# Optimization experiments

Hardware: AMD Instinct MI355X
Metric: run time of the kernel (lower is better)

Reference implementation:

```python
import jax, jax.numpy as jnp
import numpy as np
from jax import lax

DIM = 256
HEADS = 8
EPS = 1e-12  # torch F.normalize default eps
DN = ('NCHW', 'OIHW', 'NCHW')


def conv1x1(x, w):
    return lax.conv_general_dilated(x, w, (1, 1), 'VALID', dimension_numbers=DN)


def dwconv3x3(x, w):
    c = x.shape[1]
    return lax.conv_general_dilated(x, w, (1, 1), ((1, 1), (1, 1)),
                                    dimension_numbers=DN, feature_group_count=c)


def setup_inputs() -> dict:
    key = jax.random.key(0)
    ks = jax.random.split(key, 8)
    B, C, H, W = 4, DIM, 160, 160
    s = lambda fan: 1.0 / np.sqrt(fan)
    return {
        'low': jax.random.normal(ks[0], (B, C, H, W), jnp.float32),
        'high': jax.random.normal(ks[1], (B, C, H, W), jnp.float32),
        'q_w': jax.random.normal(ks[2], (C, C, 1, 1), jnp.float32) * s(C),
        'q_dw_w': jax.random.normal(ks[3], (C, 1, 3, 3), jnp.float32) * s(9),
        'kv_w': jax.random.normal(ks[4], (2 * C, C, 1, 1), jnp.float32) * s(C),
        'kv_dw_w': jax.random.normal(ks[5], (2 * C, 1, 3, 3), jnp.float32) * s(9),
        'proj_w': jax.random.normal(ks[6], (C, C, 1, 1), jnp.float32) * s(C),
        'temperature': jnp.ones((HEADS, 1, 1), jnp.float32),
    }


def reference(low, high, q_w, q_dw_w, kv_w, kv_dw_w, proj_w, temperature):
    B, C, H, W = low.shape
    hw = H * W
    ch = C // HEADS  # channels per head

    q = dwconv3x3(conv1x1(high, q_w), q_dw_w)           # [B, C, H, W]
    kv = dwconv3x3(conv1x1(low, kv_w), kv_dw_w)         # [B, 2C, H, W]
    k, v = jnp.split(kv, 2, axis=1)

    def heads(x):
        return x.reshape(B, HEADS, ch, hw)              # b head c (h w)

    q, k, v = heads(q), heads(k), heads(v)

    # L2-normalize along spatial dim (torch F.normalize semantics)
    q = q / jnp.maximum(jnp.linalg.norm(q, axis=-1, keepdims=True), EPS)
    k = k / jnp.maximum(jnp.linalg.norm(k, axis=-1, keepdims=True), EPS)

    attn = jnp.einsum('bhcn,bhdn->bhcd', q, k) * temperature  # [B, H, ch, ch]
    attn = jax.nn.softmax(attn, axis=-1)
    out = jnp.einsum('bhcd,bhdn->bhcn', attn, v)               # [B, H, ch, hw]

    out = out.reshape(B, C, H, W)
    return conv1x1(out, proj_w)
```

## Files before the change

kernel.cpp:

```cpp
#include <hip/hip_runtime.h>
#include <math.h>

#define HW 25600
#define IMGW 160
#define CDIM 256
#define NB 4
#define NHEADS 8
#define SZB ((long)CDIM * HW)

typedef __attribute__((ext_vector_type(8))) short short8v;
typedef __attribute__((ext_vector_type(4))) float f32x4;
typedef __attribute__((ext_vector_type(8))) unsigned short us8;

union FragU {
    us8 o;
    short8v s;
    unsigned u32[4];
};

__device__ inline unsigned short f2bf(float f) {
    unsigned u = __float_as_uint(f);
    return (unsigned short)((u + 0x7fffu + ((u >> 16) & 1u)) >> 16);
}
__device__ inline float bf2f(unsigned short h) {
    return __uint_as_float(((unsigned)h) << 16);
}

__global__ __launch_bounds__(256) void cvtw_k(
    const float* __restrict__ kv_w, const float* __restrict__ q_w,
    unsigned short* __restrict__ wkv_s, unsigned short* __restrict__ wq_s)
{
    int idx = blockIdx.x * 256 + threadIdx.x;
    int g2 = idx & 3;
    int kt = (idx >> 2) & 7;
    int co = idx >> 5;
    const float* src;
    unsigned short* dst;
    int nco, co_l;
    if (co < 512) { src = kv_w; dst = wkv_s; nco = 512; co_l = co; }
    else          { src = q_w;  dst = wq_s;  nco = 256; co_l = co - 512; }
    src += (long)co_l * CDIM + kt * 32 + g2 * 8;
    us8 v;
#pragma unroll
    for (int u = 0; u < 8; ++u) v[u] = f2bf(src[u]);
    int slot = g2 ^ ((co_l >> 1) & 3);
    *(us8*)(dst + ((long)kt * nco + co_l) * 32 + slot * 8) = v;
}

template<int OUTF32, int XF32>
__global__ __launch_bounds__(256) void gemm2_k(
    const void* __restrict__ Xv, const unsigned short* __restrict__ WS,
    void* __restrict__ outp, long xbs, long wbs, long obs, int nco)
{
    __shared__ __align__(16) unsigned short Wl[128 * 32];
    __shared__ __align__(16) char XBuf[XF32 ? (128 * 40 * 2) : (128 * 32 * 2)];
    unsigned short* Xl = (unsigned short*)XBuf;

    const int t  = threadIdx.x;
    const int l  = t & 63;
    const int wv = t >> 6;
    const int g  = l >> 4;
    const int ln = l & 15;

    const int NX = gridDim.x;
    const int orig = blockIdx.y * NX + blockIdx.x;
    const int chunkp = (NX * gridDim.y) >> 3;
    const int wgid = (orig & 7) * chunkp + (orig >> 3);
    const int co0 = (wgid % NX) * 128;
    const int n0  = (wgid / NX) * 128;

    const long b  = blockIdx.z;
    const unsigned short* Wb = WS + b * wbs;
    const int wr = wv >> 1, wc = wv & 1;

    f32x4 acc[4][4];
#pragma unroll
    for (int i = 0; i < 4; ++i)
#pragma unroll
        for (int j = 0; j < 4; ++j) acc[i][j] = (f32x4){0.f, 0.f, 0.f, 0.f};

    const int lrow = l >> 2;
    const int lgrp = l & 3;
    const int n_l = t & 127;
    const int sb  = (t >> 7) * 2;

    for (int kt = 0; kt < 8; ++kt) {
        __syncthreads();
#pragma unroll
        for (int ii = 0; ii < 2; ++ii) {
            int instr = wv * 2 + ii;
            int row = instr * 16 + lrow;
            const unsigned short* wsrc =
                Wb + ((long)kt * nco + co0 + row) * 32 + lgrp * 8;
            __builtin_amdgcn_global_load_lds(
                (const __attribute__((address_space(1))) void*)wsrc,
                (__attribute__((address_space(3))) void*)&Wl[instr * 512], 16, 0, 0);
        }
        if (XF32) {
            const float* Xb = (const float*)Xv + b * xbs;
#pragma unroll
            for (int si = 0; si < 2; ++si) {
                int k0 = (sb + si) * 8;
                float f[8];
#pragma unroll
                for (int u = 0; u < 8; ++u)
                    f[u] = Xb[(long)(kt * 32 + k0 + u) * HW + n0 + n_l];
                FragU cv;
#pragma unroll
                for (int e2 = 0; e2 < 4; ++e2) {
                    unsigned r;
                    asm("v_cvt_pk_bf16_f32 %0, %1, %2"
                        : "=v"(r) : "v"(f[e2 * 2]), "v"(f[e2 * 2 + 1]));
                    cv.u32[e2] = r;
                }
                *(us8*)&Xl[n_l * 40 + k0] = cv.o;
            }
        } else {
            const unsigned short* Xb = (const unsigned short*)Xv + b * xbs;
#pragma unroll
            for (int ii = 0; ii < 2; ++ii) {
                int instr = wv * 2 + ii;
                int row = instr * 16 + lrow;
                const unsigned short* xsrc =
                    Xb + ((long)kt * HW + n0 + row) * 32 + lgrp * 8;
                __builtin_amdgcn_global_load_lds(
                    (const __attribute__((address_space(1))) void*)xsrc,
                    (__attribute__((address_space(3))) void*)&Xl[instr * 512], 16, 0, 0);
            }
        }
        __syncthreads();

        FragU A_[4], B_[4];
#pragma unroll
        for (int i = 0; i < 4; ++i) {
            int row = wr * 64 + i * 16 + ln;
            int slot = g ^ ((row >> 1) & 3);
            A_[i].o = *(const us8*)&Wl[row * 32 + slot * 8];
        }
        if (XF32) {
#pragma unroll
            for (int j = 0; j < 4; ++j) {
                int row = wc * 64 + j * 16 + ln;
                B_[j].o = *(const us8*)&Xl[row * 40 + g * 8];
            }
        } else {
#pragma unroll
            for (int j = 0; j < 4; ++j) {
                int row = wc * 64 + j * 16 + ln;
                int slot = g ^ ((row >> 1) & 3);
                B_[j].o = *(const us8*)&Xl[row * 32 + slot * 8];
            }
        }
#pragma unroll
        for (int i = 0; i < 4; ++i)
#pragma unroll
            for (int j = 0; j < 4; ++j)
                acc[i][j] = __builtin_amdgcn_mfma_f32_16x16x32_bf16(
                    A_[i].s, B_[j].s, acc[i][j], 0, 0, 0);
    }

    if (OUTF32) {
        float* ob = (float*)outp + b * obs;
#pragma unroll
        for (int i = 0; i < 4; ++i)
#pragma unroll
            for (int j = 0; j < 4; ++j) {
                long ocol = n0 + wc * 64 + j * 16 + ln;
#pragma unroll
                for (int r = 0; r < 4; ++r) {
                    long orow = co0 + wr * 64 + i * 16 + g * 4 + r;
                    ob[orow * HW + ocol] = acc[i][j][r];
                }
            }
    } else {
        unsigned short* ob = (unsigned short*)outp + b * obs;
#pragma unroll
        for (int i = 0; i < 4; ++i)
#pragma unroll
            for (int j = 0; j < 4; ++j) {
                long ocol = n0 + wc * 64 + j * 16 + ln;
#pragma unroll
                for (int r = 0; r < 4; ++r) {
                    long orow = co0 + wr * 64 + i * 16 + g * 4 + r;
                    ob[orow * HW + ocol] = f2bf(acc[i][j][r]);
                }
            }
    }
}

__global__ __launch_bounds__(256) void dwK_k(
    const unsigned short* __restrict__ A, const float* __restrict__ w,
    unsigned short* __restrict__ out, long bstride)
{
    __shared__ unsigned short xsh[8][10][168];
    const int t = threadIdx.x;
    const int y0 = blockIdx.x * 8;
    const int c0 = blockIdx.y * 8;
    const long b = blockIdx.z;
    const unsigned short* Ab = A + b * bstride;

    for (int idx = t; idx < 1600; idx += 256) {
        int seg = idx % 20;
        int row = (idx / 20) % 10;
        int ch  = idx / 200;
        int yy  = y0 + row - 1;
        us8 v = (us8){0, 0, 0, 0, 0, 0, 0, 0};
        if (yy >= 0 && yy < IMGW)
            v = *(const us8*)(Ab + (long)(c0 + ch) * HW + yy * IMGW + seg * 8);
        *(us8*)&xsh[ch][row][seg * 8] = v;
    }
    __syncthreads();

    const int ch = t >> 5;
    const int rem = t & 31;
    const int ro = rem >> 2;
    const int xq = rem & 3;
    float wreg[9];
#pragma unroll
    for (int u = 0; u < 9; ++u) wreg[u] = w[(c0 + ch) * 9 + u];
    unsigned short* ob = out + b * SZB + (long)(c0 + ch) * HW + (y0 + ro) * IMGW;

#pragma unroll
    for (int xs = 0; xs < 5; ++xs) {
        int x = xq * 8 + xs * 32;
        float s[8];
#pragma unroll
        for (int p = 0; p < 8; ++p) s[p] = 0.f;
#pragma unroll
        for (int dy = 0; dy < 3; ++dy) {
            const unsigned short* rp = &xsh[ch][ro + dy][0];
            float r[10];
            r[0] = (x > 0) ? bf2f(rp[x - 1]) : 0.f;
            us8 mid = *(const us8*)&rp[x];
#pragma unroll
            for (int u = 0; u < 8; ++u) r[1 + u] = bf2f(mid[u]);
            r[9] = (x + 8 < IMGW) ? bf2f(rp[x + 8]) : 0.f;
            float w0 = wreg[dy * 3], w1 = wreg[dy * 3 + 1], w2 = wreg[dy * 3 + 2];
#pragma unroll
            for (int p = 0; p < 8; ++p)
                s[p] = fmaf(w0, r[p], fmaf(w1, r[p + 1], fmaf(w2, r[p + 2], s[p])));
        }
        us8 o;
#pragma unroll
        for (int p = 0; p < 8; ++p) o[p] = f2bf(s[p]);
        *(us8*)(ob + x) = o;
    }
}

__global__ __launch_bounds__(256) void dwV_k(
    const unsigned short* __restrict__ A, const float* __restrict__ w,
    unsigned short* __restrict__ out, long bstride)
{
    __shared__ unsigned short xsh[16][6][168];
    __shared__ unsigned short osh[640][17];
    const int t = threadIdx.x;
    const int y0 = blockIdx.x * 4;
    const int c0 = blockIdx.y * 16;
    const long b = blockIdx.z;
    const unsigned short* Ab = A + b * bstride;

    for (int idx = t; idx < 1920; idx += 256) {
        int seg = idx % 20;
        int row = (idx / 20) % 6;
        int ch  = idx / 120;
        int yy  = y0 + row - 1;
        us8 v = (us8){0, 0, 0, 0, 0, 0, 0, 0};
        if (yy >= 0 && yy < IMGW)
            v = *(const us8*)(Ab + (long)(c0 + ch) * HW + yy * IMGW + seg * 8);
        *(us8*)&xsh[ch][row][seg * 8] = v;
    }
    __syncthreads();

    {
        const int ch = t >> 4;
        const int rem = t & 15;
        const int ro = rem >> 2;
        const int xq = rem & 3;
        float wreg[9];
#pragma unroll
        for (int u = 0; u < 9; ++u) wreg[u] = w[(c0 + ch) * 9 + u];
#pragma unroll
        for (int xs = 0; xs < 5; ++xs) {
            int x = xq * 8 + xs * 32;
            float s[8];
#pragma unroll
            for (int p = 0; p < 8; ++p) s[p] = 0.f;
#pragma unroll
            for (int dy = 0; dy < 3; ++dy) {
                const unsigned short* rp = &xsh[ch][ro + dy][0];
                float r[10];
                r[0] = (x > 0) ? bf2f(rp[x - 1]) : 0.f;
                us8 mid = *(const us8*)&rp[x];
#pragma unroll
                for (int u = 0; u < 8; ++u) r[1 + u] = bf2f(mid[u]);
                r[9] = (x + 8 < IMGW) ? bf2f(rp[x + 8]) : 0.f;
                float w0 = wreg[dy * 3], w1 = wreg[dy * 3 + 1], w2 = wreg[dy * 3 + 2];
#pragma unroll
                for (int p = 0; p < 8; ++p)
                    s[p] = fmaf(w0, r[p], fmaf(w1, r[p + 1], fmaf(w2, r[p + 2], s[p])));
            }
            int nl = ro * IMGW + x;
#pragma unroll
            for (int p = 0; p < 8; ++p) osh[nl + p][ch] = f2bf(s[p]);
        }
    }
    __syncthreads();

    for (int idx = t; idx < 1280; idx += 256) {
        int nl = idx >> 1;
        int c8 = (idx & 1) * 8;
        us8 o;
#pragma unroll
        for (int u = 0; u < 8; ++u) o[u] = osh[nl][c8 + u];
        int n  = y0 * IMGW + nl;
        int cg = c0 + c8;
        int kt = cg >> 5;
        int g2 = (cg >> 3) & 3;
        int slot = g2 ^ ((n >> 1) & 3);
        *(us8*)(out + b * SZB + ((long)kt * HW + n) * 32 + slot * 8) = o;
    }
}

__global__ __launch_bounds__(256) void gram_k(
    const unsigned short* __restrict__ q, const unsigned short* __restrict__ k,
    float* __restrict__ part_qk, float* __restrict__ part_sq_q,
    float* __restrict__ part_sq_k)
{
    __shared__ float Sred[4 * 1024];
    __shared__ float sqq_l[4][32];
    __shared__ float sqk_l[4][32];
    const int t  = threadIdx.x;
    const int l  = t & 63;
    const int wv = t >> 6;
    const int g  = l >> 4;
    const int ln = l & 15;
    const int chunk = blockIdx.x;
    const int h = blockIdx.y;
    const int b = blockIdx.z;

    f32x4 accS[2][2], accQ[2], accK[2];
#pragma unroll
    for (int i = 0; i < 2; ++i) {
        accQ[i] = (f32x4){0, 0, 0, 0};
        accK[i] = (f32x4){0, 0, 0, 0};
#pragma unroll
        for (int j = 0; j < 2; ++j) accS[i][j] = (f32x4){0, 0, 0, 0};
    }

    const unsigned short* qb = q + (long)b * SZB + (long)(h * 32) * HW;
    const unsigned short* kb = k + (long)b * SZB + (long)(h * 32) * HW;
    long nb = (long)chunk * 3200 + wv * 800;
    for (int s = 0; s < 25; ++s, nb += 32) {
        FragU aq[2], bk[2];
#pragma unroll
        for (int i = 0; i < 2; ++i)
            aq[i].o = *(const us8*)(qb + (long)(i * 16 + ln) * HW + nb + g * 8);
#pragma unroll
        for (int j = 0; j < 2; ++j)
            bk[j].o = *(const us8*)(kb + (long)(j * 16 + ln) * HW + nb + g * 8);
#pragma unroll
        for (int i = 0; i < 2; ++i)
#pragma unroll
            for (int j = 0; j < 2; ++j)
                accS[i][j] = __builtin_amdgcn_mfma_f32_16x16x32_bf16(
                    aq[i].s, bk[j].s, accS[i][j], 0, 0, 0);
#pragma unroll
        for (int i = 0; i < 2; ++i) {
            accQ[i] = __builtin_amdgcn_mfma_f32_16x16x32_bf16(
                aq[i].s, aq[i].s, accQ[i], 0, 0, 0);
            accK[i] = __builtin_amdgcn_mfma_f32_16x16x32_bf16(
                bk[i].s, bk[i].s, accK[i], 0, 0, 0);
        }
    }
#pragma unroll
    for (int i = 0; i < 2; ++i)
#pragma unroll
        for (int j = 0; j < 2; ++j)
#pragma unroll
            for (int r = 0; r < 4; ++r) {
                int row = i * 16 + g * 4 + r;
                int col = j * 16 + ln;
                Sred[wv * 1024 + row * 32 + col] = accS[i][j][r];
            }
#pragma unroll
    for (int i = 0; i < 2; ++i)
#pragma unroll
        for (int r = 0; r < 4; ++r)
            if (ln == g * 4 + r) {
                sqq_l[wv][i * 16 + g * 4 + r] = accQ[i][r];
                sqk_l[wv][i * 16 + g * 4 + r] = accK[i][r];
            }
    __syncthreads();
    const long pb = ((long)(b * NHEADS + h) * 8 + chunk);
#pragma unroll
    for (int e0 = 0; e0 < 4; ++e0) {
        int e = e0 * 256 + t;
        float v = Sred[e] + Sred[1024 + e] + Sred[2048 + e] + Sred[3072 + e];
        part_qk[pb * 1024 + e] = v;
    }
    if (t < 32)
        part_sq_q[pb * 32 + t] = sqq_l[0][t] + sqq_l[1][t] + sqq_l[2][t] + sqq_l[3][t];
    else if (t < 64) {
        int j = t - 32;
        part_sq_k[pb * 32 + j] = sqk_l[0][j] + sqk_l[1][j] + sqk_l[2][j] + sqk_l[3][j];
    }
}

__global__ __launch_bounds__(256) void attn_weff_k(
    const float* __restrict__ part_qk, const float* __restrict__ part_sq_q,
    const float* __restrict__ part_sq_k, const float* __restrict__ proj_w,
    const float* __restrict__ temp, unsigned short* __restrict__ weff_s)
{
    __shared__ float at[32 * 33];
    __shared__ float nq[32], nk[32];
    int bh = blockIdx.x;
    int b = bh >> 3, h = bh & 7;
    int t = threadIdx.x;
    long pb0 = (long)bh * 8;
    float4 s = make_float4(0, 0, 0, 0);
    for (int c = 0; c < 8; ++c) {
        float4 v = *(const float4*)(part_qk + (pb0 + c) * 1024 + t * 4);
        s.x += v.x; s.y += v.y; s.z += v.z; s.w += v.w;
    }
    if (t < 32) {
        float a = 0;
        for (int c = 0; c < 8; ++c) a += part_sq_q[(pb0 + c) * 32 + t];
        nq[t] = fmaxf(sqrtf(a), 1e-12f);
    } else if (t < 64) {
        int j = t - 32;
        float a = 0;
        for (int c = 0; c < 8; ++c) a += part_sq_k[(pb0 + c) * 32 + j];
        nk[j] = fmaxf(sqrtf(a), 1e-12f);
    }
    __syncthreads();
    float tp = temp[h];
    int ci = t >> 3, cj0 = (t & 7) * 4;
    at[ci * 33 + cj0 + 0] = s.x / (nq[ci] * nk[cj0 + 0]) * tp;
    at[ci * 33 + cj0 + 1] = s.y / (nq[ci] * nk[cj0 + 1]) * tp;
    at[ci * 33 + cj0 + 2] = s.z / (nq[ci] * nk[cj0 + 2]) * tp;
    at[ci * 33 + cj0 + 3] = s.w / (nq[ci] * nk[cj0 + 3]) * tp;
    __syncthreads();
    if (t < 32) {
        float m = -1e30f;
        for (int j = 0; j < 32; ++j) m = fmaxf(m, at[t * 33 + j]);
        float ss = 0;
        for (int j = 0; j < 32; ++j) {
            float e = expf(at[t * 33 + j] - m);
            at[t * 33 + j] = e;
            ss += e;
        }
        float inv = 1.f / ss;
        for (int j = 0; j < 32; ++j) at[t * 33 + j] *= inv;
    }
    __syncthreads();
    int co = t;
    float pw[32];
#pragma unroll
    for (int i2 = 0; i2 < 32; ++i2) pw[i2] = proj_w[(long)co * CDIM + h * 32 + i2];
    unsigned short* wb = weff_s + (long)b * 65536 + (long)h * (256 * 32) + co * 32;
    int swz = (co >> 1) & 3;
    for (int j = 0; j < 32; ++j) {
        float a = 0;
#pragma unroll
        for (int i2 = 0; i2 < 32; ++i2) a = fmaf(pw[i2], at[i2 * 33 + j], a);
        wb[((j >> 3) ^ swz) * 8 + (j & 7)] = f2bf(a);
    }
}

extern "C" void kernel_launch(void* const* d_in, const int* in_sizes, int n_in,
                              void* d_out, int out_size, void* d_ws, size_t ws_size,
                              hipStream_t stream)
{
    const float* low    = (const float*)d_in[0];
    const float* high   = (const float*)d_in[1];
    const float* q_w    = (const float*)d_in[2];
    const float* q_dw   = (const float*)d_in[3];
    const float* kv_w   = (const float*)d_in[4];
    const float* kv_dw  = (const float*)d_in[5];
    const float* proj_w = (const float*)d_in[6];
    const float* temp   = (const float*)d_in[7];
    float* out = (float*)d_out;

    unsigned short* usws = (unsigned short*)d_ws;
    unsigned short* Areg = usws;
    unsigned short* VT   = Areg + 8 * SZB;
    unsigned short* wkv_s = VT + 4 * SZB;
    unsigned short* wq_s  = wkv_s + 131072;
    unsigned short* weff_s = wq_s + 65536;
    float* part_qk   = (float*)(weff_s + 4L * 65536);
    float* part_sq_q = part_qk + 32L * 8 * 1024;
    float* part_sq_k = part_sq_q + 32L * 8 * 32;
    float* endp      = part_sq_k + 32L * 8 * 32;
    if (ws_size < (size_t)((char*)endp - (char*)d_ws)) return;

    unsigned short* K_all = (unsigned short*)d_out;
    unsigned short* Q_all = K_all + 4 * SZB;

    dim3 blk(256);

    cvtw_k<<<dim3(96), blk, 0, stream>>>(kv_w, q_w, wkv_s, wq_s);

    gemm2_k<0, 1><<<dim3(4, 200, NB), blk, 0, stream>>>(
        low, wkv_s, Areg, SZB, 0, 2 * SZB, 512);
    dwK_k<<<dim3(20, 32, NB), blk, 0, stream>>>(Areg, kv_dw, K_all, 2 * SZB);
    dwV_k<<<dim3(40, 16, NB), blk, 0, stream>>>(Areg + 256L * HW,
                                                kv_dw + 256 * 9, VT, 2 * SZB);

    gemm2_k<0, 1><<<dim3(2, 200, NB), blk, 0, stream>>>(
        high, wq_s, Areg, SZB, 0, 2 * SZB, 256);
    dwK_k<<<dim3(20, 32, NB), blk, 0, stream>>>(Areg, q_dw, Q_all, 2 * SZB);

    gram_k<<<dim3(8, NHEADS, NB), blk, 0, stream>>>(Q_all, K_all, part_qk,
                                                    part_sq_q, part_sq_k);
    attn_weff_k<<<dim3(32), blk, 0, stream>>>(
        part_qk, part_sq_q, part_sq_k, proj_w, temp, weff_s);

    gemm2_k<1, 0><<<dim3(2, 200, NB), blk, 0, stream>>>(VT, weff_s, out,
                                                        SZB, 65536, SZB, 256);
}
```

Measured before the change: 308.2 us.

## Double-buffer GEMM LDS staging and stage epilogue through shared memory

```diff
diff --git a/kernel.cpp b/kernel.cpp
--- a/kernel.cpp
+++ b/kernel.cpp
@@ -48,13 +48,14 @@
 }
 
 template<int OUTF32, int XF32>
-__global__ __launch_bounds__(256) void gemm2_k(
+__global__ __launch_bounds__(256) void gemm3_k(
     const void* __restrict__ Xv, const unsigned short* __restrict__ WS,
     void* __restrict__ outp, long xbs, long wbs, long obs, int nco)
 {
-    __shared__ __align__(16) unsigned short Wl[128 * 32];
-    __shared__ __align__(16) char XBuf[XF32 ? (128 * 40 * 2) : (128 * 32 * 2)];
-    unsigned short* Xl = (unsigned short*)XBuf;
+    __shared__ __align__(16) char SMEM[36864];
+    unsigned short* Wl = (unsigned short*)SMEM;
+    unsigned short* Xl = (unsigned short*)(SMEM + 16384);
+    const int XST = XF32 ? 5120 : 4096;
 
     const int t  = threadIdx.x;
     const int l  = t & 63;
@@ -70,7 +71,9 @@
     const int n0  = (wgid / NX) * 128;
 
     const long b  = blockIdx.z;
-    const unsigned short* Wb = WS + b * wbs;
+    const unsigned short* Wb  = WS + b * wbs;
+    const float* Xfp          = (const float*)Xv + b * xbs;
+    const unsigned short* Xbf = (const unsigned short*)Xv + b * xbs;
     const int wr = wv >> 1, wc = wv & 1;
 
     f32x4 acc[4][4];
@@ -84,71 +87,93 @@
     const int n_l = t & 127;
     const int sb  = (t >> 7) * 2;
 
+    float f[16];
+
+#define STAGE_W(ktv, buf)                                                     \
+    {                                                                         \
+        _Pragma("unroll")                                                     \
+        for (int ii = 0; ii < 2; ++ii) {                                      \
+            int instr = wv * 2 + ii;                                          \
+            int row = instr * 16 + lrow;                                      \
+            const unsigned short* wsrc =                                      \
+                Wb + ((long)(ktv) * nco + co0 + row) * 32 + lgrp * 8;         \
+            __builtin_amdgcn_global_load_lds(                                 \
+                (const __attribute__((address_space(1))) void*)wsrc,          \
+                (__attribute__((address_space(3))) void*)                     \
+                    &Wl[(buf) * 4096 + instr * 512], 16, 0, 0);               \
+        }                                                                     \
+    }
+#define STAGE_XG(ktv, buf)                                                    \
+    {                                                                         \
+        _Pragma("unroll")                                                     \
+        for (int ii = 0; ii < 2; ++ii) {                                      \
+            int instr = wv * 2 + ii;                                          \
+            int row = instr * 16 + lrow;                                      \
+            const unsigned short* xsrc =                                      \
+                Xbf + ((long)(ktv) * HW + n0 + row) * 32 + lgrp * 8;          \
+            __builtin_amdgcn_global_load_lds(                                 \
+                (const __attribute__((address_space(1))) void*)xsrc,          \
+                (__attribute__((address_space(3))) void*)                     \
+                    &Xl[(buf) * 4096 + instr * 512], 16, 0, 0);               \
+        }                                                                     \
+    }
+#define LOAD_XF(ktv)                                                          \
+    {                                                                         \
+        _Pragma("unroll")                                                     \
+        for (int si = 0; si < 2; ++si)                                        \
+            _Pragma("unroll")                                                 \
+            for (int u = 0; u < 8; ++u)                                       \
+                f[si * 8 + u] =                                               \
+                    Xfp[(long)((ktv) * 32 + (sb + si) * 8 + u) * HW + n0 + n_l]; \
+    }
+#define WRITE_XF(buf)                                                         \
+    {                                                                         \
+        _Pragma("unroll")                                                     \
+        for (int si = 0; si < 2; ++si) {                                      \
+            FragU cv;                                                         \
+            _Pragma("unroll")                                                 \
+            for (int e2 = 0; e2 < 4; ++e2) {                                  \
+                unsigned rr;                                                  \
+                asm("v_cvt_pk_bf16_f32 %0, %1, %2"                            \
+                    : "=v"(rr) : "v"(f[si * 8 + e2 * 2]),                     \
+                      "v"(f[si * 8 + e2 * 2 + 1]));                           \
+                cv.u32[e2] = rr;                                              \
+            }                                                                 \
+            *(us8*)&Xl[(buf) * XST + n_l * 40 + (sb + si) * 8] = cv.o;        \
+        }                                                                     \
+    }
+
+    STAGE_W(0, 0);
+    if (XF32) { LOAD_XF(0); WRITE_XF(0); }
+    else      { STAGE_XG(0, 0); }
+    __syncthreads();
+
     for (int kt = 0; kt < 8; ++kt) {
-        __syncthreads();
-#pragma unroll
-        for (int ii = 0; ii < 2; ++ii) {
-            int instr = wv * 2 + ii;
-            int row = instr * 16 + lrow;
-            const unsigned short* wsrc =
-                Wb + ((long)kt * nco + co0 + row) * 32 + lgrp * 8;
-            __builtin_amdgcn_global_load_lds(
-                (const __attribute__((address_space(1))) void*)wsrc,
-                (__attribute__((address_space(3))) void*)&Wl[instr * 512], 16, 0, 0);
-        }
-        if (XF32) {
-            const float* Xb = (const float*)Xv + b * xbs;
-#pragma unroll
-            for (int si = 0; si < 2; ++si) {
-                int k0 = (sb + si) * 8;
-                float f[8];
-#pragma unroll
-                for (int u = 0; u < 8; ++u)
-                    f[u] = Xb[(long)(kt * 32 + k0 + u) * HW + n0 + n_l];
-                FragU cv;
-#pragma unroll
-                for (int e2 = 0; e2 < 4; ++e2) {
-                    unsigned r;
-                    asm("v_cvt_pk_bf16_f32 %0, %1, %2"
-                        : "=v"(r) : "v"(f[e2 * 2]), "v"(f[e2 * 2 + 1]));
-                    cv.u32[e2] = r;
-                }
-                *(us8*)&Xl[n_l * 40 + k0] = cv.o;
-            }
-        } else {
-            const unsigned short* Xb = (const unsigned short*)Xv + b * xbs;
-#pragma unroll
-            for (int ii = 0; ii < 2; ++ii) {
-                int instr = wv * 2 + ii;
-                int row = instr * 16 + lrow;
-                const unsigned short* xsrc =
-                    Xb + ((long)kt * HW + n0 + row) * 32 + lgrp * 8;
-                __builtin_amdgcn_global_load_lds(
-                    (const __attribute__((address_space(1))) void*)xsrc,
-                    (__attribute__((address_space(3))) void*)&Xl[instr * 512], 16, 0, 0);
-            }
-        }
-        __syncthreads();
-
+        const int cur = kt & 1, nxt = cur ^ 1;
+        if (kt < 7) {
+            STAGE_W(kt + 1, nxt);
+            if (XF32) { LOAD_XF(kt + 1); }
+            else      { STAGE_XG(kt + 1, nxt); }
+        }
         FragU A_[4], B_[4];
 #pragma unroll
         for (int i = 0; i < 4; ++i) {
             int row = wr * 64 + i * 16 + ln;
             int slot = g ^ ((row >> 1) & 3);
-            A_[i].o = *(const us8*)&Wl[row * 32 + slot * 8];
+            A_[i].o = *(const us8*)&Wl[cur * 4096 + row * 32 + slot * 8];
         }
         if (XF32) {
 #pragma unroll
             for (int j = 0; j < 4; ++j) {
                 int row = wc * 64 + j * 16 + ln;
-                B_[j].o = *(const us8*)&Xl[row * 40 + g * 8];
+                B_[j].o = *(const us8*)&Xl[cur * XST + row * 40 + g * 8];
             }
         } else {
 #pragma unroll
             for (int j = 0; j < 4; ++j) {
                 int row = wc * 64 + j * 16 + ln;
                 int slot = g ^ ((row >> 1) & 3);
-                B_[j].o = *(const us8*)&Xl[row * 32 + slot * 8];
+                B_[j].o = *(const us8*)&Xl[cur * XST + row * 32 + slot * 8];
             }
         }
 #pragma unroll
@@ -157,34 +182,60 @@
             for (int j = 0; j < 4; ++j)
                 acc[i][j] = __builtin_amdgcn_mfma_f32_16x16x32_bf16(
                     A_[i].s, B_[j].s, acc[i][j], 0, 0, 0);
-    }
+        if (kt < 7 && XF32) { WRITE_XF(nxt); }
+        __syncthreads();
+    }
+#undef STAGE_W
+#undef STAGE_XG
+#undef LOAD_XF
+#undef WRITE_XF
 
     if (OUTF32) {
+        float* ef = (float*)SMEM;
         float* ob = (float*)outp + b * obs;
 #pragma unroll
+        for (int h2 = 0; h2 < 2; ++h2) {
+            if (wr == h2) {
+#pragma unroll
+                for (int i = 0; i < 4; ++i)
+#pragma unroll
+                    for (int j = 0; j < 4; ++j)
+#pragma unroll
+                        for (int r = 0; r < 4; ++r)
+                            ef[(i * 16 + g * 4 + r) * 132 + wc * 64 + j * 16 + ln]
+                                = acc[i][j][r];
+            }
+            __syncthreads();
+#pragma unroll
+            for (int p = 0; p < 8; ++p) {
+                int idx = p * 256 + t;
+                int row = idx >> 5;
+                int c4 = (idx & 31) * 4;
+                float4 v = *(const float4*)&ef[row * 132 + c4];
+                *(float4*)(ob + (long)(co0 + h2 * 64 + row) * HW + n0 + c4) = v;
+            }
+            __syncthreads();
+        }
+    } else {
+        unsigned short* eb = (unsigned short*)SMEM;
+        unsigned short* ob = (unsigned short*)outp + b * obs;
+#pragma unroll
         for (int i = 0; i < 4; ++i)
 #pragma unroll
-            for (int j = 0; j < 4; ++j) {
-                long ocol = n0 + wc * 64 + j * 16 + ln;
-#pragma unroll
-                for (int r = 0; r < 4; ++r) {
-                    long orow = co0 + wr * 64 + i * 16 + g * 4 + r;
-                    ob[orow * HW + ocol] = acc[i][j][r];
-                }
-            }
-    } else {
-        unsigned short* ob = (unsigned short*)outp + b * obs;
-#pragma unroll
-        for (int i = 0; i < 4; ++i)
-#pragma unroll
-            for (int j = 0; j < 4; ++j) {
-                long ocol = n0 + wc * 64 + j * 16 + ln;
-#pragma unroll
-                for (int r = 0; r < 4; ++r) {
-                    long orow = co0 + wr * 64 + i * 16 + g * 4 + r;
-                    ob[orow * HW + ocol] = f2bf(acc[i][j][r]);
-                }
-            }
+            for (int j = 0; j < 4; ++j)
+#pragma unroll
+                for (int r = 0; r < 4; ++r)
+                    eb[(wr * 64 + i * 16 + g * 4 + r) * 136 + wc * 64 + j * 16 + ln]
+                        = f2bf(acc[i][j][r]);
+        __syncthreads();
+#pragma unroll
+        for (int p = 0; p < 8; ++p) {
+            int idx = p * 256 + t;
+            int row = idx >> 4;
+            int c8 = (idx & 15) * 8;
+            us8 v = *(const us8*)&eb[row * 136 + c8];
+            *(us8*)(ob + (long)(co0 + row) * HW + n0 + c8) = v;
+        }
     }
 }
 
@@ -500,13 +551,13 @@
 
     cvtw_k<<<dim3(96), blk, 0, stream>>>(kv_w, q_w, wkv_s, wq_s);
 
-    gemm2_k<0, 1><<<dim3(4, 200, NB), blk, 0, stream>>>(
+    gemm3_k<0, 1><<<dim3(4, 200, NB), blk, 0, stream>>>(
         low, wkv_s, Areg, SZB, 0, 2 * SZB, 512);
     dwK_k<<<dim3(20, 32, NB), blk, 0, stream>>>(Areg, kv_dw, K_all, 2 * SZB);
     dwV_k<<<dim3(40, 16, NB), blk, 0, stream>>>(Areg + 256L * HW,
                                                 kv_dw + 256 * 9, VT, 2 * SZB);
 
-    gemm2_k<0, 1><<<dim3(2, 200, NB), blk, 0, stream>>>(
+    gemm3_k<0, 1><<<dim3(2, 200, NB), blk, 0, stream>>>(
         high, wq_s, Areg, SZB, 0, 2 * SZB, 256);
     dwK_k<<<dim3(20, 32, NB), blk, 0, stream>>>(Areg, q_dw, Q_all, 2 * SZB);
 
@@ -515,6 +566,6 @@
     attn_weff_k<<<dim3(32), blk, 0, stream>>>(
         part_qk, part_sq_q, part_sq_k, proj_w, temp, weff_s);
 
-    gemm2_k<1, 0><<<dim3(2, 200, NB), blk, 0, stream>>>(VT, weff_s, out,
+    gemm3_k<1, 0><<<dim3(2, 200, NB), blk, 0, stream>>>(VT, weff_s, out,
                                                         SZB, 65536, SZB, 256);
 }
```

After: 288.7 us. 6.3% less time.

## Load GEMM fragments directly from global memory and stage epilogue through LDS

Applied to the files above, without the earlier changes.

```diff
diff --git a/kernel.cpp b/kernel.cpp
--- a/kernel.cpp
+++ b/kernel.cpp
@@ -28,34 +28,27 @@
 
 __global__ __launch_bounds__(256) void cvtw_k(
     const float* __restrict__ kv_w, const float* __restrict__ q_w,
-    unsigned short* __restrict__ wkv_s, unsigned short* __restrict__ wq_s)
-{
-    int idx = blockIdx.x * 256 + threadIdx.x;
-    int g2 = idx & 3;
-    int kt = (idx >> 2) & 7;
-    int co = idx >> 5;
+    unsigned short* __restrict__ wkv, unsigned short* __restrict__ wq)
+{
+    long i = ((long)blockIdx.x * 256 + threadIdx.x) * 8;
     const float* src;
     unsigned short* dst;
-    int nco, co_l;
-    if (co < 512) { src = kv_w; dst = wkv_s; nco = 512; co_l = co; }
-    else          { src = q_w;  dst = wq_s;  nco = 256; co_l = co - 512; }
-    src += (long)co_l * CDIM + kt * 32 + g2 * 8;
-    us8 v;
-#pragma unroll
-    for (int u = 0; u < 8; ++u) v[u] = f2bf(src[u]);
-    int slot = g2 ^ ((co_l >> 1) & 3);
-    *(us8*)(dst + ((long)kt * nco + co_l) * 32 + slot * 8) = v;
+    if (i < 131072) { src = kv_w + i; dst = wkv + i; }
+    else            { src = q_w + (i - 131072); dst = wq + (i - 131072); }
+    float4 v0 = *(const float4*)src;
+    float4 v1 = *(const float4*)(src + 4);
+    us8 o;
+    o[0] = f2bf(v0.x); o[1] = f2bf(v0.y); o[2] = f2bf(v0.z); o[3] = f2bf(v0.w);
+    o[4] = f2bf(v1.x); o[5] = f2bf(v1.y); o[6] = f2bf(v1.z); o[7] = f2bf(v1.w);
+    *(us8*)dst = o;
 }
 
 template<int OUTF32, int XF32>
-__global__ __launch_bounds__(256) void gemm2_k(
-    const void* __restrict__ Xv, const unsigned short* __restrict__ WS,
-    void* __restrict__ outp, long xbs, long wbs, long obs, int nco)
-{
-    __shared__ __align__(16) unsigned short Wl[128 * 32];
-    __shared__ __align__(16) char XBuf[XF32 ? (128 * 40 * 2) : (128 * 32 * 2)];
-    unsigned short* Xl = (unsigned short*)XBuf;
-
+__global__ __launch_bounds__(256) void gemm5_k(
+    const void* __restrict__ Xv, const unsigned short* __restrict__ W,
+    void* __restrict__ outp, long xbs, long wbs, long obs)
+{
+    __shared__ __align__(16) char SMEM[34816];
     const int t  = threadIdx.x;
     const int l  = t & 63;
     const int wv = t >> 6;
@@ -70,8 +63,12 @@
     const int n0  = (wgid / NX) * 128;
 
     const long b  = blockIdx.z;
-    const unsigned short* Wb = WS + b * wbs;
+    const unsigned short* Wb  = W + b * wbs;
+    const float* Xfp          = (const float*)Xv + b * xbs;
+    const unsigned short* Xbf = (const unsigned short*)Xv + b * xbs;
     const int wr = wv >> 1, wc = wv & 1;
+    const int arow0 = co0 + wr * 64 + ln;
+    const int bcol0 = n0 + wc * 64 + ln;
 
     f32x4 acc[4][4];
 #pragma unroll
@@ -79,77 +76,31 @@
 #pragma unroll
         for (int j = 0; j < 4; ++j) acc[i][j] = (f32x4){0.f, 0.f, 0.f, 0.f};
 
-    const int lrow = l >> 2;
-    const int lgrp = l & 3;
-    const int n_l = t & 127;
-    const int sb  = (t >> 7) * 2;
-
     for (int kt = 0; kt < 8; ++kt) {
-        __syncthreads();
-#pragma unroll
-        for (int ii = 0; ii < 2; ++ii) {
-            int instr = wv * 2 + ii;
-            int row = instr * 16 + lrow;
-            const unsigned short* wsrc =
-                Wb + ((long)kt * nco + co0 + row) * 32 + lgrp * 8;
-            __builtin_amdgcn_global_load_lds(
-                (const __attribute__((address_space(1))) void*)wsrc,
-                (__attribute__((address_space(3))) void*)&Wl[instr * 512], 16, 0, 0);
-        }
+        const int kb = kt * 32 + g * 8;
+        FragU A_[4], B_[4];
+#pragma unroll
+        for (int i = 0; i < 4; ++i)
+            A_[i].o = *(const us8*)&Wb[(long)(arow0 + i * 16) * CDIM + kb];
         if (XF32) {
-            const float* Xb = (const float*)Xv + b * xbs;
-#pragma unroll
-            for (int si = 0; si < 2; ++si) {
-                int k0 = (sb + si) * 8;
+#pragma unroll
+            for (int j = 0; j < 4; ++j) {
                 float f[8];
 #pragma unroll
                 for (int u = 0; u < 8; ++u)
-                    f[u] = Xb[(long)(kt * 32 + k0 + u) * HW + n0 + n_l];
-                FragU cv;
+                    f[u] = Xfp[(long)(kb + u) * HW + bcol0 + j * 16];
 #pragma unroll
                 for (int e2 = 0; e2 < 4; ++e2) {
-                    unsigned r;
+                    unsigned rr;
                     asm("v_cvt_pk_bf16_f32 %0, %1, %2"
-                        : "=v"(r) : "v"(f[e2 * 2]), "v"(f[e2 * 2 + 1]));
-                    cv.u32[e2] = r;
+                        : "=v"(rr) : "v"(f[e2 * 2]), "v"(f[e2 * 2 + 1]));
+                    B_[j].u32[e2] = rr;
                 }
-                *(us8*)&Xl[n_l * 40 + k0] = cv.o;
             }
         } else {
-            const unsigned short* Xb = (const unsigned short*)Xv + b * xbs;
-#pragma unroll
-            for (int ii = 0; ii < 2; ++ii) {
-                int instr = wv * 2 + ii;
-                int row = instr * 16 + lrow;
-                const unsigned short* xsrc =
-                    Xb + ((long)kt * HW + n0 + row) * 32 + lgrp * 8;
-                __builtin_amdgcn_global_load_lds(
-                    (const __attribute__((address_space(1))) void*)xsrc,
-                    (__attribute__((address_space(3))) void*)&Xl[instr * 512], 16, 0, 0);
-            }
-        }
-        __syncthreads();
-
-        FragU A_[4], B_[4];
-#pragma unroll
-        for (int i = 0; i < 4; ++i) {
-            int row = wr * 64 + i * 16 + ln;
-            int slot = g ^ ((row >> 1) & 3);
-            A_[i].o = *(const us8*)&Wl[row * 32 + slot * 8];
-        }
-        if (XF32) {
-#pragma unroll
-            for (int j = 0; j < 4; ++j) {
-                int row = wc * 64 + j * 16 + ln;
-                B_[j].o = *(const us8*)&Xl[row * 40 + g * 8];
-            }
-        } else {
-#pragma unroll
-            for (int j = 0; j < 4; ++j) {
-                int row = wc * 64 + j * 16 + ln;
-                int slot = g ^ ((row >> 1) & 3);
-                B_[j].o = *(const us8*)&Xl[row * 32 + slot * 8];
-            }
+#pragma unroll
+            for (int j = 0; j < 4; ++j)
+                B_[j].o = *(const us8*)&Xbf[(long)(bcol0 + j * 16) * CDIM + kb];
         }
 #pragma unroll
         for (int i = 0; i < 4; ++i)
@@ -160,31 +111,51 @@
     }
 
     if (OUTF32) {
+        float* ef = (float*)SMEM;
         float* ob = (float*)outp + b * obs;
 #pragma unroll
+        for (int h2 = 0; h2 < 2; ++h2) {
+            if (wr == h2) {
+#pragma unroll
+                for (int i = 0; i < 4; ++i)
+#pragma unroll
+                    for (int j = 0; j < 4; ++j)
+#pragma unroll
+                        for (int r = 0; r < 4; ++r)
+                            ef[(i * 16 + g * 4 + r) * 132 + wc * 64 + j * 16 + ln]
+                                = acc[i][j][r];
+            }
+            __syncthreads();
+#pragma unroll
+            for (int p = 0; p < 8; ++p) {
+                int idx = p * 256 + t;
+                int row = idx >> 5;
+                int c4 = (idx & 31) * 4;
+                float4 v = *(const float4*)&ef[row * 132 + c4];
+                *(float4*)(ob + (long)(co0 + h2 * 64 + row) * HW + n0 + c4) = v;
+            }
+            __syncthreads();
+        }
+    } else {
+        unsigned short* eb = (unsigned short*)SMEM;
+        unsigned short* ob = (unsigned short*)outp + b * obs;
+#pragma unroll
         for (int i = 0; i < 4; ++i)
 #pragma unroll
-            for (int j = 0; j < 4; ++j) {
-                long ocol = n0 + wc * 64 + j * 16 + ln;
-#pragma unroll
-                for (int r = 0; r < 4; ++r) {
-                    long orow = co0 + wr * 64 + i * 16 + g * 4 + r;
-                    ob[orow * HW + ocol] = acc[i][j][r];
-                }
-            }
-    } else {
-        unsigned short* ob = (unsigned short*)outp + b * obs;
-#pragma unroll
-        for (int i = 0; i < 4; ++i)
-#pragma unroll
-            for (int j = 0; j < 4; ++j) {
-                long ocol = n0 + wc * 64 + j * 16 + ln;
-#pragma unroll
-                for (int r = 0; r < 4; ++r) {
-                    long orow = co0 + wr * 64 + i * 16 + g * 4 + r;
-                    ob[orow * HW + ocol] = f2bf(acc[i][j][r]);
-                }
-            }
+            for (int j = 0; j < 4; ++j)
+#pragma unroll
+                for (int r = 0; r < 4; ++r)
+                    eb[(wr * 64 + i * 16 + g * 4 + r) * 136 + wc * 64 + j * 16 + ln]
+                        = f2bf(acc[i][j][r]);
+        __syncthreads();
+#pragma unroll
+        for (int p = 0; p < 8; ++p) {
+            int idx = p * 256 + t;
+            int row = idx >> 4;
+            int c8 = (idx & 15) * 8;
+            us8 v = *(const us8*)&eb[row * 136 + c8];
+            *(us8*)(ob + (long)(co0 + row) * HW + n0 + c8) = v;
+        }
     }
 }
 
@@ -312,12 +283,8 @@
         us8 o;
 #pragma unroll
         for (int u = 0; u < 8; ++u) o[u] = osh[nl][c8 + u];
-        int n  = y0 * IMGW + nl;
-        int cg = c0 + c8;
-        int kt = cg >> 5;
-        int g2 = (cg >> 3) & 3;
-        int slot = g2 ^ ((n >> 1) & 3);
-        *(us8*)(out + b * SZB + ((long)kt * HW + n) * 32 + slot * 8) = o;
+        long n = y0 * IMGW + nl;
+        *(us8*)(out + b * SZB + n * CDIM + c0 + c8) = o;
     }
 }
 
@@ -409,7 +376,7 @@
 __global__ __launch_bounds__(256) void attn_weff_k(
     const float* __restrict__ part_qk, const float* __restrict__ part_sq_q,
     const float* __restrict__ part_sq_k, const float* __restrict__ proj_w,
-    const float* __restrict__ temp, unsigned short* __restrict__ weff_s)
+    const float* __restrict__ temp, unsigned short* __restrict__ weff)
 {
     __shared__ float at[32 * 33];
     __shared__ float nq[32], nk[32];
@@ -457,13 +424,12 @@
     float pw[32];
 #pragma unroll
     for (int i2 = 0; i2 < 32; ++i2) pw[i2] = proj_w[(long)co * CDIM + h * 32 + i2];
-    unsigned short* wb = weff_s + (long)b * 65536 + (long)h * (256 * 32) + co * 32;
-    int swz = (co >> 1) & 3;
+    unsigned short* wb = weff + (long)b * 65536 + (long)co * CDIM + h * 32;
     for (int j = 0; j < 32; ++j) {
         float a = 0;
 #pragma unroll
         for (int i2 = 0; i2 < 32; ++i2) a = fmaf(pw[i2], at[i2 * 33 + j], a);
-        wb[((j >> 3) ^ swz) * 8 + (j & 7)] = f2bf(a);
+        wb[j] = f2bf(a);
     }
 }
 
@@ -484,10 +450,10 @@
     unsigned short* usws = (unsigned short*)d_ws;
     unsigned short* Areg = usws;
     unsigned short* VT   = Areg + 8 * SZB;
-    unsigned short* wkv_s = VT + 4 * SZB;
-    unsigned short* wq_s  = wkv_s + 131072;
-    unsigned short* weff_s = wq_s + 65536;
-    float* part_qk   = (float*)(weff_s + 4L * 65536);
+    unsigned short* wkv_p = VT + 4 * SZB;
+    unsigned short* wq_p  = wkv_p + 131072;
+    unsigned short* weff_p = wq_p + 65536;
+    float* part_qk   = (float*)(weff_p + 4L * 65536);
     float* part_sq_q = part_qk + 32L * 8 * 1024;
     float* part_sq_k = part_sq_q + 32L * 8 * 32;
     float* endp      = part_sq_k + 32L * 8 * 32;
@@ -498,23 +464,23 @@
 
     dim3 blk(256);
 
-    cvtw_k<<<dim3(96), blk, 0, stream>>>(kv_w, q_w, wkv_s, wq_s);
-
-    gemm2_k<0, 1><<<dim3(4, 200, NB), blk, 0, stream>>>(
-        low, wkv_s, Areg, SZB, 0, 2 * SZB, 512);
+    cvtw_k<<<dim3(96), blk, 0, stream>>>(kv_w, q_w, wkv_p, wq_p);
+
+    gemm5_k<0, 1><<<dim3(4, 200, NB), blk, 0, stream>>>(
+        low, wkv_p, Areg, SZB, 0, 2 * SZB);
     dwK_k<<<dim3(20, 32, NB), blk, 0, stream>>>(Areg, kv_dw, K_all, 2 * SZB);
     dwV_k<<<dim3(40, 16, NB), blk, 0, stream>>>(Areg + 256L * HW,
                                                 kv_dw + 256 * 9, VT, 2 * SZB);
 
-    gemm2_k<0, 1><<<dim3(2, 200, NB), blk, 0, stream>>>(
-        high, wq_s, Areg, SZB, 0, 2 * SZB, 256);
+    gemm5_k<0, 1><<<dim3(2, 200, NB), blk, 0, stream>>>(
+        high, wq_p, Areg, SZB, 0, 2 * SZB);
     dwK_k<<<dim3(20, 32, NB), blk, 0, stream>>>(Areg, q_dw, Q_all, 2 * SZB);
 
     gram_k<<<dim3(8, NHEADS, NB), blk, 0, stream>>>(Q_all, K_all, part_qk,
                                                     part_sq_q, part_sq_k);
     attn_weff_k<<<dim3(32), blk, 0, stream>>>(
-        part_qk, part_sq_q, part_sq_k, proj_w, temp, weff_s);
-
-    gemm2_k<1, 0><<<dim3(2, 200, NB), blk, 0, stream>>>(VT, weff_s, out,
-                                                        SZB, 65536, SZB, 256);
-}
+        part_qk, part_sq_q, part_sq_k, proj_w, temp, weff_p);
+
+    gemm5_k<1, 0><<<dim3(2, 200, NB), blk, 0, stream>>>(VT, weff_p, out,
+                                                        SZB, 65536, SZB);
+}
```

Result: slower. 374.3 us (+21.4%).
